# Optimization experiments

Hardware: AMD Instinct MI355X
Metric: run time of the kernel (lower is better)

Reference implementation:

```python
import jax, jax.numpy as jnp
import numpy as np
import math

B, S, D, H = 2, 2048, 1024, 16
DK = D // H  # 64
THETA = 500000.0


def setup_inputs() -> dict:
    key = jax.random.key(0)
    ks = jax.random.split(key, 6)
    x = jax.random.normal(ks[0], (B, S, D), dtype=jnp.float32)
    # RoPE frequencies: inv_freq = theta^{-(2i/dk)}, angles = pos * inv_freq
    inv_freq = 1.0 / (THETA ** (jnp.arange(0, DK, 2, dtype=jnp.float32) / DK))  # [DK/2]
    angles = jnp.arange(S, dtype=jnp.float32)[:, None] * inv_freq[None, :]      # [S, DK/2]
    freqs_cos = jnp.cos(angles)
    freqs_sin = jnp.sin(angles)
    # causal additive mask [B, S, S]: 0 on/below diagonal, -1e9 above
    causal = jnp.tril(jnp.ones((S, S), dtype=bool))
    mask = jnp.where(causal, 0.0, -1e9).astype(jnp.float32)
    mask = jnp.broadcast_to(mask, (B, S, S))
    scale = 0.02
    wq = jax.random.normal(ks[1], (D, D), dtype=jnp.float32) * scale
    wk = jax.random.normal(ks[2], (D, D), dtype=jnp.float32) * scale
    wv = jax.random.normal(ks[3], (D, D), dtype=jnp.float32) * scale
    wo = jax.random.normal(ks[4], (D, D), dtype=jnp.float32) * scale
    return {"x": x, "freqs_cos": freqs_cos, "freqs_sin": freqs_sin,
            "mask": mask, "wq": wq, "wk": wk, "wv": wv, "wo": wo}


def _apply_rope(t, cos, sin):
    # t: [B, S, H, DK]; cos/sin: [S, DK/2]
    tr = t.reshape(*t.shape[:-1], DK // 2, 2)
    t0, t1 = tr[..., 0], tr[..., 1]
    c = cos[None, :, None, :]
    s = sin[None, :, None, :]
    out = jnp.stack([t0 * c - t1 * s, t0 * s + t1 * c], axis=-1)
    return out.reshape(*t.shape)


def reference(x, freqs_cos, freqs_sin, mask, wq, wk, wv, wo):
    b, s, d = x.shape
    # nn.Linear(bias=False): y = x @ W^T, W is [out, in]
    q = jnp.einsum('bsd,ed->bse', x, wq).reshape(b, s, H, DK)
    k = jnp.einsum('bsd,ed->bse', x, wk).reshape(b, s, H, DK)
    v = jnp.einsum('bsd,ed->bse', x, wv).reshape(b, s, H, DK)
    q = _apply_rope(q, freqs_cos, freqs_sin)
    k = _apply_rope(k, freqs_cos, freqs_sin)
    inv_sqrt_dk = 1.0 / math.sqrt(DK)
    # scores: [B, H, S, S]
    scores = jnp.einsum('bqhd,bkhd->bhqk', q, k) * inv_sqrt_dk
    scores = scores + mask[:, None, :, :]
    # NOTE: the original module divides by sqrt(d_k) a SECOND time before softmax
    attn = jax.nn.softmax(scores * inv_sqrt_dk, axis=-1)
    out = jnp.einsum('bhqk,bkhd->bqhd', attn, v).reshape(b, s, d)
    return jnp.einsum('bsd,ed->bse', out, wo)
```

## Files before the change

kernel.cpp:

```cpp
#include <hip/hip_runtime.h>
#include <stdint.h>

#define Bq 2
#define Sq 2048
#define Dq 1024
#define Hq 16
#define DKq 64

typedef unsigned short u16;
typedef __attribute__((ext_vector_type(8))) __bf16 bf8;
typedef __attribute__((ext_vector_type(4))) __bf16 bf4;
typedef __attribute__((ext_vector_type(4))) float fx4;
typedef __attribute__((ext_vector_type(8))) unsigned short us8;
typedef __attribute__((ext_vector_type(4))) unsigned short us4;

__device__ __forceinline__ u16 f2bf(float f) {
    union { float f; unsigned int i; } v; v.f = f;
    unsigned int r = v.i + 0x7FFFu + ((v.i >> 16) & 1u);
    return (u16)(r >> 16);
}

__device__ __forceinline__ void gll16(const void* g, void* l) {
    typedef __attribute__((address_space(1))) void GV;
    typedef __attribute__((address_space(3))) void LV;
    __builtin_amdgcn_global_load_lds((GV*)g, (LV*)l, 16, 0, 0);
}

template<int N> __device__ __forceinline__ void waitv() {
    asm volatile("s_waitcnt vmcnt(%0)" :: "n"(N) : "memory");
}
__device__ __forceinline__ void SB() { __builtin_amdgcn_sched_barrier(0); }

__global__ void __launch_bounds__(256) cvt_all(const float* __restrict__ x,
                                               const float* __restrict__ wq,
                                               const float* __restrict__ wk,
                                               const float* __restrict__ wv,
                                               const float* __restrict__ wo,
                                               u16* __restrict__ ws) {
    int blk = blockIdx.x;
    const float* s;
    u16* d;
    int i;
    if (blk < 4096)      { s = x;  d = ws;           i = blk * 256 + threadIdx.x; }
    else if (blk < 5120) { s = wq; d = ws + 4194304; i = (blk - 4096) * 256 + threadIdx.x; }
    else if (blk < 6144) { s = wk; d = ws + 5242880; i = (blk - 5120) * 256 + threadIdx.x; }
    else if (blk < 7168) { s = wv; d = ws + 6291456; i = (blk - 6144) * 256 + threadIdx.x; }
    else                 { s = wo; d = ws + 7340032; i = (blk - 7168) * 256 + threadIdx.x; }
    float4 v = *(const float4*)(s + (size_t)i * 4);
    us4 o;
    o[0] = f2bf(v.x); o[1] = f2bf(v.y); o[2] = f2bf(v.z); o[3] = f2bf(v.w);
    *(us4*)(d + (size_t)i * 4) = o;
}

template<int MODE>
__global__ void __launch_bounds__(512, 4) gemm_bt(
    const u16* __restrict__ A,
    const u16* __restrict__ W0, const u16* __restrict__ W1, const u16* __restrict__ W2,
    u16* __restrict__ O0, u16* __restrict__ O1, u16* __restrict__ O2,
    float* __restrict__ Of,
    const float* __restrict__ fc, const float* __restrict__ fs)
{
    constexpr int K = 1024;
    constexpr int NT = 32;
    constexpr int BN = MODE ? 256 : 128;
    constexpr int WN = BN / 4;
    constexpr int NJ = WN / 16;
    constexpr int BOPS = BN / 128;
    constexpr int SOPS = 1 + BOPS;
    constexpr int ASZ = 128 * 32;
    constexpr int BSZ = BN * 32;
    __shared__ __align__(16) u16 As[3 * ASZ];
    __shared__ __align__(16) u16 Bs[3 * BSZ];
    const int tid = threadIdx.x;
    const int lane = tid & 63, wid = tid >> 6;
    const int wr = wid >> 2, wc = wid & 3;
    const int fr = lane & 15, fq = lane >> 4;

    int wgid = blockIdx.x;
    int Xc = wgid & 7, jj = wgid >> 3;
    int by, bx, bz;
    if (MODE == 1) {
        int T = Xc * 48 + jj;
        by = T / 12;
        int p = T - by * 12;
        bz = p >> 2; bx = p & 3;
    } else {
        int T = Xc * 32 + jj;
        by = T >> 3; bx = T & 7; bz = 0;
    }
    const int m0 = by * 128, n0 = bx * BN;

    const u16* Wm = W0;
    u16* Ob = O0;
    if (MODE == 1) {
        if (bz == 1)      { Wm = W1; Ob = O1; }
        else if (bz == 2) { Wm = W2; Ob = O2; }
    }

    const int arow = tid >> 2;
    const int scol = (((tid & 3) ^ (arow & 3)) * 8);
    const u16* ga = A  + (size_t)(m0 + arow) * K + scol;
    const u16* gb = Wm + (size_t)(n0 + arow) * K + scol;

    fx4 acc[4][NJ] = {};

    auto STAGE = [&](int t, int b) {
        gll16(ga + t * 32, As + b * ASZ + tid * 8);
        #pragma unroll
        for (int c = 0; c < BOPS; ++c)
            gll16(gb + (size_t)c * 128 * K + t * 32, Bs + b * BSZ + c * 4096 + tid * 8);
    };

    const int kq = (fq ^ (fr & 3)) * 8;

    STAGE(0, 0); STAGE(1, 1); STAGE(2, 2);
    waitv<2 * SOPS>();
    SB(); __builtin_amdgcn_s_barrier(); SB();

    #pragma unroll 1
    for (int t = 0; t < NT; ++t) {
        const u16* Ab = As + (t % 3) * ASZ;
        const u16* Bb = Bs + (t % 3) * BSZ;
        bf8 af[4], bf[NJ];
        #pragma unroll
        for (int mi = 0; mi < 4; ++mi)
            af[mi] = *(const bf8*)(&Ab[(wr * 64 + mi * 16 + fr) * 32 + kq]);
        #pragma unroll
        for (int nj = 0; nj < NJ; ++nj)
            bf[nj] = *(const bf8*)(&Bb[(wc * WN + nj * 16 + fr) * 32 + kq]);
        if (t + 2 < NT) STAGE(t + 2, (t + 2) % 3);
        __builtin_amdgcn_s_setprio(1);
        #pragma unroll
        for (int mi = 0; mi < 4; ++mi)
            #pragma unroll
            for (int nj = 0; nj < NJ; ++nj)
                acc[mi][nj] = __builtin_amdgcn_mfma_f32_16x16x32_bf16(af[mi], bf[nj], acc[mi][nj], 0, 0, 0);
        __builtin_amdgcn_s_setprio(0);
        SB();
        if (t < NT - 2)       { waitv<SOPS>(); }
        else if (t == NT - 2) { waitv<0>(); }
        SB(); __builtin_amdgcn_s_barrier(); SB();
    }

    if (MODE == 0) {
        #pragma unroll
        for (int mi = 0; mi < 4; ++mi)
            #pragma unroll
            for (int nj = 0; nj < NJ; ++nj)
                #pragma unroll
                for (int r = 0; r < 4; ++r) {
                    int m = m0 + wr * 64 + mi * 16 + fq * 4 + r;
                    int n = n0 + wc * WN + nj * 16 + fr;
                    Of[(size_t)m * 1024 + n] = acc[mi][nj][r];
                }
    } else if (bz == 2) {
        #pragma unroll
        for (int mi = 0; mi < 4; ++mi)
            #pragma unroll
            for (int nj = 0; nj < NJ; ++nj) {
                int n = n0 + wc * WN + nj * 16 + fr;
                int mb = m0 + wr * 64 + mi * 16 + fq * 4;
                int b = mb >> 11, s = mb & 2047;
                int h = n >> 6, dk = n & 63;
                bf4 pk;
                #pragma unroll
                for (int r = 0; r < 4; ++r) pk[r] = (__bf16)acc[mi][nj][r];
                *(bf4*)((__bf16*)Ob + (((size_t)(b * Hq + h)) * DKq + dk) * Sq + s) = pk;
            }
    } else {
        #pragma unroll
        for (int mi = 0; mi < 4; ++mi)
            #pragma unroll
            for (int nj = 0; nj < NJ; ++nj) {
                int n = n0 + wc * WN + nj * 16 + fr;
                int h = n >> 6, dk = n & 63;
                int ip = dk >> 1;
                float sgn = (dk & 1) ? 1.f : -1.f;
                #pragma unroll
                for (int r = 0; r < 4; ++r) {
                    int m = m0 + wr * 64 + mi * 16 + fq * 4 + r;
                    int b = m >> 11, s = m & 2047;
                    float v = acc[mi][nj][r];
                    float pv = __shfl_xor(v, 1);
                    float c  = fc[s * 32 + ip];
                    float sn = fs[s * 32 + ip];
                    float o = v * c + sgn * pv * sn;
                    ((__bf16*)Ob)[(((size_t)(b * Hq + h)) * Sq + s) * DKq + dk] = (__bf16)o;
                }
            }
    }
}

__device__ __forceinline__ int swz(int row) { return ((row & 7) ^ ((row >> 3) & 7)) << 4; }

__global__ void __launch_bounds__(512, 4) attn_k(const u16* __restrict__ Q,
                                                 const u16* __restrict__ Kg,
                                                 const u16* __restrict__ Vtg,
                                                 u16* __restrict__ AO) {
    int L = blockIdx.x + 32 * blockIdx.y;
    int X = L & 7, C = L >> 3;
    const int bh = X * 4 + (C & 3);
    const int Qt = 31 - (C >> 2);
    const int b = bh >> 4, h = bh & 15;
    const int tid = threadIdx.x, lane = tid & 63, wid = tid >> 6;
    const int wq4 = wid & 3, par = wid >> 2;
    const int fr = lane & 15, fq = lane >> 4;
    const int swzfr = swz(fr);

    __shared__ __align__(16) u16 Ks[2][64 * 64];
    __shared__ __align__(16) u16 Vs[2][64 * 64];
    __shared__ __align__(16) u16 Ps[8][16 * 64];
    __shared__ float Lx[4][64];

    const u16* Kp = Kg  + (size_t)bh * Sq * 64;
    const u16* Vp = Vtg + (size_t)bh * 64 * Sq;
    const int q0 = Qt * 64;
    const int nt = Qt + 1;
    const int NS = (nt + 1) >> 1;

    bf8 qf0, qf1;
    {
        const u16* Qp = Q + ((size_t)bh * Sq + q0) * 64;
        int qr = wq4 * 16 + fr;
        qf0 = *(const bf8*)(Qp + qr * 64 + fq * 8);
        qf1 = *(const bf8*)(Qp + qr * 64 + fq * 8 + 32);
    }

    fx4 oacc[4] = {};
    float l_loc = 0.f;

    const int srow = tid >> 3;
    const int sce  = (tid & 7) * 8;
    const int ldst = srow * 128 + (((tid & 7) * 16) ^ swz(srow));

    us8 kreg[2], vreg[2];
    #pragma unroll
    for (int c = 0; c < 2; ++c) {
        int t = c < nt ? c : nt - 1;
        kreg[c] = *(const us8*)(Kp + ((size_t)t * 64 + srow) * 64 + sce);
        vreg[c] = *(const us8*)(Vp + (size_t)srow * Sq + t * 64 + sce);
    }
    #pragma unroll
    for (int c = 0; c < 2; ++c) {
        *(us8*)((char*)Ks[c] + ldst) = kreg[c];
        *(us8*)((char*)Vs[c] + ldst) = vreg[c];
    }
    if (NS > 1) {
        #pragma unroll
        for (int c = 0; c < 2; ++c) {
            int t = 2 + c < nt ? 2 + c : nt - 1;
            kreg[c] = *(const us8*)(Kp + ((size_t)t * 64 + srow) * 64 + sce);
            vreg[c] = *(const us8*)(Vp + (size_t)srow * Sq + t * 64 + sce);
        }
    }
    __syncthreads();

    #pragma unroll 1
    for (int sp = 0; sp < NS; ++sp) {
        const int t = 2 * sp + par;
        if (t < nt) {
            const char* Kb = (const char*)Ks[par];
            const char* Vb = (const char*)Vs[par];
            char* Pw = (char*)Ps[wid] + fr * 128;

            fx4 sf[4];
            __builtin_amdgcn_s_setprio(1);
            #pragma unroll
            for (int sj = 0; sj < 4; ++sj) {
                int krow = sj * 16 + fr;
                bf8 kf0 = *(const bf8*)(Kb + krow * 128 + ((fq * 16) ^ swz(krow)));
                bf8 kf1 = *(const bf8*)(Kb + krow * 128 + ((64 + fq * 16) ^ swz(krow)));
                fx4 a = {0.f, 0.f, 0.f, 0.f};
                a = __builtin_amdgcn_mfma_f32_16x16x32_bf16(kf0, qf0, a, 0, 0, 0);
                a = __builtin_amdgcn_mfma_f32_16x16x32_bf16(kf1, qf1, a, 0, 0, 0);
                sf[sj] = a;
            }
            __builtin_amdgcn_s_setprio(0);

            float pv[4][4];
            #pragma unroll
            for (int sj = 0; sj < 4; ++sj)
                #pragma unroll
                for (int r = 0; r < 4; ++r)
                    pv[sj][r] = __expf(sf[sj][r] * 0.015625f);
            if (t == Qt) {
                int ql = wq4 * 16 + fr;
                #pragma unroll
                for (int sj = 0; sj < 4; ++sj)
                    #pragma unroll
                    for (int r = 0; r < 4; ++r)
                        if (sj * 16 + fq * 4 + r > ql) pv[sj][r] = 0.f;
            }
            #pragma unroll
            for (int sj = 0; sj < 4; ++sj) {
                bf4 w;
                #pragma unroll
                for (int r = 0; r < 4; ++r) { w[r] = (__bf16)pv[sj][r]; l_loc += pv[sj][r]; }
                *(bf4*)(Pw + ((sj * 32 + fq * 8) ^ swzfr)) = w;
            }

            __builtin_amdgcn_s_setprio(1);
            #pragma unroll
            for (int kk = 0; kk < 2; ++kk) {
                bf8 pf = *(const bf8*)(Pw + ((kk * 64 + fq * 16) ^ swzfr));
                #pragma unroll
                for (int mf = 0; mf < 4; ++mf) {
                    int vrow = mf * 16 + fr;
                    bf8 vf = *(const bf8*)(Vb + vrow * 128 + ((kk * 64 + fq * 16) ^ swz(vrow)));
                    oacc[mf] = __builtin_amdgcn_mfma_f32_16x16x32_bf16(vf, pf, oacc[mf], 0, 0, 0);
                }
            }
            __builtin_amdgcn_s_setprio(0);
        }
        __syncthreads();
        if (sp + 1 < NS) {
            #pragma unroll
            for (int c = 0; c < 2; ++c) {
                *(us8*)((char*)Ks[c] + ldst) = kreg[c];
                *(us8*)((char*)Vs[c] + ldst) = vreg[c];
            }
            if (sp + 2 < NS) {
                #pragma unroll
                for (int c = 0; c < 2; ++c) {
                    int tt = 2 * (sp + 2) + c; if (tt > nt - 1) tt = nt - 1;
                    kreg[c] = *(const us8*)(Kp + ((size_t)tt * 64 + srow) * 64 + sce);
                    vreg[c] = *(const us8*)(Vp + (size_t)srow * Sq + tt * 64 + sce);
                }
            }
            __syncthreads();
        }
    }

    l_loc += __shfl_xor(l_loc, 16);
    l_loc += __shfl_xor(l_loc, 32);
    if (par == 1) {
        float* ob = (float*)Ps + wq4 * 1024;
        #pragma unroll
        for (int mf = 0; mf < 4; ++mf)
            *(fx4*)(ob + lane * 16 + mf * 4) = oacc[mf];
        Lx[wq4][lane] = l_loc;
    }
    __syncthreads();
    if (par == 0) {
        const float* ob = (float*)Ps + wq4 * 1024;
        float lt = l_loc + Lx[wq4][lane];
        float linv = __builtin_amdgcn_rcpf(lt);
        int s = q0 + wq4 * 16 + fr;
        #pragma unroll
        for (int mf = 0; mf < 4; ++mf) {
            fx4 oh = *(const fx4*)(ob + lane * 16 + mf * 4);
            bf4 pk;
            #pragma unroll
            for (int r = 0; r < 4; ++r) pk[r] = (__bf16)((oacc[mf][r] + oh[r]) * linv);
            *(bf4*)((__bf16*)AO + ((size_t)(b * Sq + s)) * Dq + h * 64 + mf * 16 + fq * 4) = pk;
        }
    }
}

extern "C" void kernel_launch(void* const* d_in, const int* in_sizes, int n_in,
                              void* d_out, int out_size, void* d_ws, size_t ws_size,
                              hipStream_t stream) {
    const float* x  = (const float*)d_in[0];
    const float* fc = (const float*)d_in[1];
    const float* fs = (const float*)d_in[2];
    const float* wq = (const float*)d_in[4];
    const float* wk = (const float*)d_in[5];
    const float* wv = (const float*)d_in[6];
    const float* wo = (const float*)d_in[7];
    float* out = (float*)d_out;

    u16* ws  = (u16*)d_ws;
    u16* xb  = ws;
    u16* wqb = ws + 4194304;
    u16* wkb = ws + 5242880;
    u16* wvb = ws + 6291456;
    u16* wob = ws + 7340032;
    u16* Qb  = ws + 8388608;
    u16* Kb  = ws + 12582912;
    u16* Vb  = ws + 16777216;
    u16* AOb = ws + 20971520;

    cvt_all<<<8192, 256, 0, stream>>>(x, wq, wk, wv, wo, ws);

    gemm_bt<1><<<384, 512, 0, stream>>>(xb, wqb, wkb, wvb, Qb, Kb, Vb, nullptr, fc, fs);

    dim3 g2(32, 32, 1);
    attn_k<<<g2, 512, 0, stream>>>(Qb, Kb, Vb, AOb);

    gemm_bt<0><<<256, 512, 0, stream>>>(AOb, wob, nullptr, nullptr, nullptr, nullptr, nullptr, out, nullptr, nullptr);
}
```

Before: 104.7 us.

## Double query tile per attention block to reuse K/V tiles across two query groups

```diff
diff --git a/kernel.cpp b/kernel.cpp
--- a/kernel.cpp
+++ b/kernel.cpp
@@ -197,37 +197,41 @@
                                                  const u16* __restrict__ Kg,
                                                  const u16* __restrict__ Vtg,
                                                  u16* __restrict__ AO) {
-    int L = blockIdx.x + 32 * blockIdx.y;
-    int X = L & 7, C = L >> 3;
-    const int bh = X * 4 + (C & 3);
-    const int Qt = 31 - (C >> 2);
+    int j = blockIdx.x;
+    int Xc = j & 7;
+    int lightHalf = j >> 8;
+    int C = (j >> 3) & 31;
+    const int bh = Xc * 4 + (C & 3);
+    const int Qt = lightHalf ? (C >> 2) : (15 - (C >> 2));
     const int b = bh >> 4, h = bh & 15;
     const int tid = threadIdx.x, lane = tid & 63, wid = tid >> 6;
-    const int wq4 = wid & 3, par = wid >> 2;
+    const int qh = wid & 3, par = wid >> 2;
     const int fr = lane & 15, fq = lane >> 4;
-    const int swzfr = swz(fr);
+    const int swq0 = ((fr & 7) ^ ((fr >> 3) & 7)) << 4;
+    const int swq1 = ((fr & 7) ^ (((fr >> 3) + 2) & 7)) << 4;
 
     __shared__ __align__(16) u16 Ks[2][64 * 64];
     __shared__ __align__(16) u16 Vs[2][64 * 64];
-    __shared__ __align__(16) u16 Ps[8][16 * 64];
-    __shared__ float Lx[4][64];
+    __shared__ __align__(16) u16 Ps[8][32 * 64];
+    __shared__ float Lx[2][4][64];
 
     const u16* Kp = Kg  + (size_t)bh * Sq * 64;
     const u16* Vp = Vtg + (size_t)bh * 64 * Sq;
-    const int q0 = Qt * 64;
-    const int nt = Qt + 1;
-    const int NS = (nt + 1) >> 1;
-
-    bf8 qf0, qf1;
+    const int q0 = Qt * 128;
+    const int NS = Qt + 1;
+    const int qwb = q0 + qh * 32;
+
+    bf8 qf00, qf01, qf10, qf11;
     {
-        const u16* Qp = Q + ((size_t)bh * Sq + q0) * 64;
-        int qr = wq4 * 16 + fr;
-        qf0 = *(const bf8*)(Qp + qr * 64 + fq * 8);
-        qf1 = *(const bf8*)(Qp + qr * 64 + fq * 8 + 32);
-    }
-
-    fx4 oacc[4] = {};
-    float l_loc = 0.f;
+        const u16* Qp = Q + ((size_t)bh * Sq + qwb) * 64;
+        qf00 = *(const bf8*)(Qp + fr * 64 + fq * 8);
+        qf01 = *(const bf8*)(Qp + fr * 64 + fq * 8 + 32);
+        qf10 = *(const bf8*)(Qp + (16 + fr) * 64 + fq * 8);
+        qf11 = *(const bf8*)(Qp + (16 + fr) * 64 + fq * 8 + 32);
+    }
+
+    fx4 oacc[2][4] = {};
+    float l0 = 0.f, l1 = 0.f;
 
     const int srow = tid >> 3;
     const int sce  = (tid & 7) * 8;
@@ -236,9 +240,8 @@
     us8 kreg[2], vreg[2];
     #pragma unroll
     for (int c = 0; c < 2; ++c) {
-        int t = c < nt ? c : nt - 1;
-        kreg[c] = *(const us8*)(Kp + ((size_t)t * 64 + srow) * 64 + sce);
-        vreg[c] = *(const us8*)(Vp + (size_t)srow * Sq + t * 64 + sce);
+        kreg[c] = *(const us8*)(Kp + ((size_t)c * 64 + srow) * 64 + sce);
+        vreg[c] = *(const us8*)(Vp + (size_t)srow * Sq + c * 64 + sce);
     }
     #pragma unroll
     for (int c = 0; c < 2; ++c) {
@@ -248,9 +251,8 @@
     if (NS > 1) {
         #pragma unroll
         for (int c = 0; c < 2; ++c) {
-            int t = 2 + c < nt ? 2 + c : nt - 1;
-            kreg[c] = *(const us8*)(Kp + ((size_t)t * 64 + srow) * 64 + sce);
-            vreg[c] = *(const us8*)(Vp + (size_t)srow * Sq + t * 64 + sce);
+            kreg[c] = *(const us8*)(Kp + ((size_t)(2 + c) * 64 + srow) * 64 + sce);
+            vreg[c] = *(const us8*)(Vp + (size_t)srow * Sq + (2 + c) * 64 + sce);
         }
     }
     __syncthreads();
@@ -258,59 +260,63 @@
     #pragma unroll 1
     for (int sp = 0; sp < NS; ++sp) {
         const int t = 2 * sp + par;
-        if (t < nt) {
+        if (t * 64 <= qwb + 31) {
             const char* Kb = (const char*)Ks[par];
             const char* Vb = (const char*)Vs[par];
-            char* Pw = (char*)Ps[wid] + fr * 128;
-
-            fx4 sf[4];
-            __builtin_amdgcn_s_setprio(1);
+            char* Pw = (char*)Ps[wid];
+            const int base = qwb - t * 64;
+            const bool dg = (base < 63);
+
             #pragma unroll
             for (int sj = 0; sj < 4; ++sj) {
                 int krow = sj * 16 + fr;
                 bf8 kf0 = *(const bf8*)(Kb + krow * 128 + ((fq * 16) ^ swz(krow)));
                 bf8 kf1 = *(const bf8*)(Kb + krow * 128 + ((64 + fq * 16) ^ swz(krow)));
-                fx4 a = {0.f, 0.f, 0.f, 0.f};
-                a = __builtin_amdgcn_mfma_f32_16x16x32_bf16(kf0, qf0, a, 0, 0, 0);
-                a = __builtin_amdgcn_mfma_f32_16x16x32_bf16(kf1, qf1, a, 0, 0, 0);
-                sf[sj] = a;
-            }
-            __builtin_amdgcn_s_setprio(0);
-
-            float pv[4][4];
-            #pragma unroll
-            for (int sj = 0; sj < 4; ++sj)
-                #pragma unroll
-                for (int r = 0; r < 4; ++r)
-                    pv[sj][r] = __expf(sf[sj][r] * 0.015625f);
-            if (t == Qt) {
-                int ql = wq4 * 16 + fr;
-                #pragma unroll
-                for (int sj = 0; sj < 4; ++sj)
+                __builtin_amdgcn_s_setprio(1);
+                fx4 s0 = {0.f, 0.f, 0.f, 0.f}, s1 = {0.f, 0.f, 0.f, 0.f};
+                s0 = __builtin_amdgcn_mfma_f32_16x16x32_bf16(kf0, qf00, s0, 0, 0, 0);
+                s0 = __builtin_amdgcn_mfma_f32_16x16x32_bf16(kf1, qf01, s0, 0, 0, 0);
+                s1 = __builtin_amdgcn_mfma_f32_16x16x32_bf16(kf0, qf10, s1, 0, 0, 0);
+                s1 = __builtin_amdgcn_mfma_f32_16x16x32_bf16(kf1, qf11, s1, 0, 0, 0);
+                __builtin_amdgcn_s_setprio(0);
+                float p0[4], p1[4];
+                #pragma unroll
+                for (int r = 0; r < 4; ++r) {
+                    p0[r] = __expf(s0[r] * 0.015625f);
+                    p1[r] = __expf(s1[r] * 0.015625f);
+                }
+                if (dg) {
                     #pragma unroll
-                    for (int r = 0; r < 4; ++r)
-                        if (sj * 16 + fq * 4 + r > ql) pv[sj][r] = 0.f;
-            }
-            #pragma unroll
-            for (int sj = 0; sj < 4; ++sj) {
-                bf4 w;
-                #pragma unroll
-                for (int r = 0; r < 4; ++r) { w[r] = (__bf16)pv[sj][r]; l_loc += pv[sj][r]; }
-                *(bf4*)(Pw + ((sj * 32 + fq * 8) ^ swzfr)) = w;
-            }
-
-            __builtin_amdgcn_s_setprio(1);
+                    for (int r = 0; r < 4; ++r) {
+                        int kvr = sj * 16 + fq * 4 + r;
+                        if (kvr > base + fr)      p0[r] = 0.f;
+                        if (kvr > base + 16 + fr) p1[r] = 0.f;
+                    }
+                }
+                bf4 w0, w1;
+                #pragma unroll
+                for (int r = 0; r < 4; ++r) {
+                    w0[r] = (__bf16)p0[r]; l0 += p0[r];
+                    w1[r] = (__bf16)p1[r]; l1 += p1[r];
+                }
+                *(bf4*)(Pw + fr * 128 + ((sj * 32 + fq * 8) ^ swq0)) = w0;
+                *(bf4*)(Pw + (16 + fr) * 128 + ((sj * 32 + fq * 8) ^ swq1)) = w1;
+            }
+
             #pragma unroll
             for (int kk = 0; kk < 2; ++kk) {
-                bf8 pf = *(const bf8*)(Pw + ((kk * 64 + fq * 16) ^ swzfr));
+                bf8 pf0 = *(const bf8*)(Pw + fr * 128 + ((kk * 64 + fq * 16) ^ swq0));
+                bf8 pf1 = *(const bf8*)(Pw + (16 + fr) * 128 + ((kk * 64 + fq * 16) ^ swq1));
+                __builtin_amdgcn_s_setprio(1);
                 #pragma unroll
                 for (int mf = 0; mf < 4; ++mf) {
                     int vrow = mf * 16 + fr;
                     bf8 vf = *(const bf8*)(Vb + vrow * 128 + ((kk * 64 + fq * 16) ^ swz(vrow)));
-                    oacc[mf] = __builtin_amdgcn_mfma_f32_16x16x32_bf16(vf, pf, oacc[mf], 0, 0, 0);
-                }
-            }
-            __builtin_amdgcn_s_setprio(0);
+                    oacc[0][mf] = __builtin_amdgcn_mfma_f32_16x16x32_bf16(vf, pf0, oacc[0][mf], 0, 0, 0);
+                    oacc[1][mf] = __builtin_amdgcn_mfma_f32_16x16x32_bf16(vf, pf1, oacc[1][mf], 0, 0, 0);
+                }
+                __builtin_amdgcn_s_setprio(0);
+            }
         }
         __syncthreads();
         if (sp + 1 < NS) {
@@ -322,7 +328,7 @@
             if (sp + 2 < NS) {
                 #pragma unroll
                 for (int c = 0; c < 2; ++c) {
-                    int tt = 2 * (sp + 2) + c; if (tt > nt - 1) tt = nt - 1;
+                    int tt = 2 * (sp + 2) + c;
                     kreg[c] = *(const us8*)(Kp + ((size_t)tt * 64 + srow) * 64 + sce);
                     vreg[c] = *(const us8*)(Vp + (size_t)srow * Sq + tt * 64 + sce);
                 }
@@ -331,28 +337,38 @@
         }
     }
 
-    l_loc += __shfl_xor(l_loc, 16);
-    l_loc += __shfl_xor(l_loc, 32);
+    l0 += __shfl_xor(l0, 16); l0 += __shfl_xor(l0, 32);
+    l1 += __shfl_xor(l1, 16); l1 += __shfl_xor(l1, 32);
     if (par == 1) {
-        float* ob = (float*)Ps + wq4 * 1024;
-        #pragma unroll
-        for (int mf = 0; mf < 4; ++mf)
-            *(fx4*)(ob + lane * 16 + mf * 4) = oacc[mf];
-        Lx[wq4][lane] = l_loc;
+        float* pb = (float*)Ps + qh * 2048;
+        #pragma unroll
+        for (int qs = 0; qs < 2; ++qs)
+            #pragma unroll
+            for (int mf = 0; mf < 4; ++mf) {
+                int slot = (qs * 4 + mf) ^ (lane & 7);
+                *(fx4*)(pb + lane * 32 + slot * 4) = oacc[qs][mf];
+            }
+        Lx[0][qh][lane] = l0;
+        Lx[1][qh][lane] = l1;
     }
     __syncthreads();
     if (par == 0) {
-        const float* ob = (float*)Ps + wq4 * 1024;
-        float lt = l_loc + Lx[wq4][lane];
-        float linv = __builtin_amdgcn_rcpf(lt);
-        int s = q0 + wq4 * 16 + fr;
-        #pragma unroll
-        for (int mf = 0; mf < 4; ++mf) {
-            fx4 oh = *(const fx4*)(ob + lane * 16 + mf * 4);
-            bf4 pk;
-            #pragma unroll
-            for (int r = 0; r < 4; ++r) pk[r] = (__bf16)((oacc[mf][r] + oh[r]) * linv);
-            *(bf4*)((__bf16*)AO + ((size_t)(b * Sq + s)) * Dq + h * 64 + mf * 16 + fq * 4) = pk;
+        const float* pb = (const float*)Ps + qh * 2048;
+        float li0 = __builtin_amdgcn_rcpf(l0 + Lx[0][qh][lane]);
+        float li1 = __builtin_amdgcn_rcpf(l1 + Lx[1][qh][lane]);
+        #pragma unroll
+        for (int qs = 0; qs < 2; ++qs) {
+            float li = qs ? li1 : li0;
+            int s = q0 + qh * 32 + qs * 16 + fr;
+            #pragma unroll
+            for (int mf = 0; mf < 4; ++mf) {
+                int slot = (qs * 4 + mf) ^ (lane & 7);
+                fx4 oh = *(const fx4*)(pb + lane * 32 + slot * 4);
+                bf4 pk;
+                #pragma unroll
+                for (int r = 0; r < 4; ++r) pk[r] = (__bf16)((oacc[qs][mf][r] + oh[r]) * li);
+                *(bf4*)((__bf16*)AO + ((size_t)(b * Sq + s)) * Dq + h * 64 + mf * 16 + fq * 4) = pk;
+            }
         }
     }
 }
@@ -384,8 +400,7 @@
 
     gemm_bt<1><<<384, 512, 0, stream>>>(xb, wqb, wkb, wvb, Qb, Kb, Vb, nullptr, fc, fs);
 
-    dim3 g2(32, 32, 1);
-    attn_k<<<g2, 512, 0, stream>>>(Qb, Kb, Vb, AOb);
+    attn_k<<<512, 512, 0, stream>>>(Qb, Kb, Vb, AOb);
 
     gemm_bt<0><<<256, 512, 0, stream>>>(AOb, wob, nullptr, nullptr, nullptr, nullptr, nullptr, out, nullptr, nullptr);
 }
```

New measurement: 144.5 us. +37.9%, slower.

## Fuse fp32-to-bf16 conversion of x into the QKV projection GEMM

Applied to the files above, without the earlier changes.

```diff
diff --git a/kernel.cpp b/kernel.cpp
--- a/kernel.cpp
+++ b/kernel.cpp
@@ -31,21 +31,19 @@
 }
 __device__ __forceinline__ void SB() { __builtin_amdgcn_sched_barrier(0); }
 
-__global__ void __launch_bounds__(256) cvt_all(const float* __restrict__ x,
-                                               const float* __restrict__ wq,
-                                               const float* __restrict__ wk,
-                                               const float* __restrict__ wv,
-                                               const float* __restrict__ wo,
-                                               u16* __restrict__ ws) {
+__global__ void __launch_bounds__(256) cvt_w(const float* __restrict__ wq,
+                                             const float* __restrict__ wk,
+                                             const float* __restrict__ wv,
+                                             const float* __restrict__ wo,
+                                             u16* __restrict__ ws) {
     int blk = blockIdx.x;
     const float* s;
     u16* d;
     int i;
-    if (blk < 4096)      { s = x;  d = ws;           i = blk * 256 + threadIdx.x; }
-    else if (blk < 5120) { s = wq; d = ws + 4194304; i = (blk - 4096) * 256 + threadIdx.x; }
-    else if (blk < 6144) { s = wk; d = ws + 5242880; i = (blk - 5120) * 256 + threadIdx.x; }
-    else if (blk < 7168) { s = wv; d = ws + 6291456; i = (blk - 6144) * 256 + threadIdx.x; }
-    else                 { s = wo; d = ws + 7340032; i = (blk - 7168) * 256 + threadIdx.x; }
+    if (blk < 1024)      { s = wq; d = ws + 4194304; i = blk * 256 + threadIdx.x; }
+    else if (blk < 2048) { s = wk; d = ws + 5242880; i = (blk - 1024) * 256 + threadIdx.x; }
+    else if (blk < 3072) { s = wv; d = ws + 6291456; i = (blk - 2048) * 256 + threadIdx.x; }
+    else                 { s = wo; d = ws + 7340032; i = (blk - 3072) * 256 + threadIdx.x; }
     float4 v = *(const float4*)(s + (size_t)i * 4);
     us4 o;
     o[0] = f2bf(v.x); o[1] = f2bf(v.y); o[2] = f2bf(v.z); o[3] = f2bf(v.w);
@@ -54,7 +52,7 @@
 
 template<int MODE>
 __global__ void __launch_bounds__(512, 4) gemm_bt(
-    const u16* __restrict__ A,
+    const u16* __restrict__ A, const float* __restrict__ Af,
     const u16* __restrict__ W0, const u16* __restrict__ W1, const u16* __restrict__ W2,
     u16* __restrict__ O0, u16* __restrict__ O1, u16* __restrict__ O2,
     float* __restrict__ Of,
@@ -66,7 +64,6 @@
     constexpr int WN = BN / 4;
     constexpr int NJ = WN / 16;
     constexpr int BOPS = BN / 128;
-    constexpr int SOPS = 1 + BOPS;
     constexpr int ASZ = 128 * 32;
     constexpr int BSZ = BN * 32;
     __shared__ __align__(16) u16 As[3 * ASZ];
@@ -98,47 +95,82 @@
     }
 
     const int arow = tid >> 2;
-    const int scol = (((tid & 3) ^ (arow & 3)) * 8);
-    const u16* ga = A  + (size_t)(m0 + arow) * K + scol;
-    const u16* gb = Wm + (size_t)(n0 + arow) * K + scol;
+    const int sw = ((tid & 3) ^ (arow & 3)) * 8;
+    const u16*   ga  = A  + (size_t)(m0 + arow) * K + sw;
+    const float* gaf = Af + (size_t)(m0 + arow) * K + (tid & 3) * 8;
+    const u16*   gb  = Wm + (size_t)(n0 + arow) * K + sw;
 
     fx4 acc[4][NJ] = {};
 
-    auto STAGE = [&](int t, int b) {
-        gll16(ga + t * 32, As + b * ASZ + tid * 8);
+    auto STAGE_B = [&](int t, int b) {
         #pragma unroll
         for (int c = 0; c < BOPS; ++c)
             gll16(gb + (size_t)c * 128 * K + t * 32, Bs + b * BSZ + c * 4096 + tid * 8);
     };
+    auto STAGE_A0 = [&](int t, int b) {
+        gll16(ga + t * 32, As + b * ASZ + tid * 8);
+    };
+    float4 xra, xrb;
+    auto LOAD_X = [&](int t) {
+        xra = *(const float4*)(gaf + t * 32);
+        xrb = *(const float4*)(gaf + t * 32 + 4);
+    };
+    auto WRITE_A = [&](int b) {
+        us8 w;
+        w[0] = f2bf(xra.x); w[1] = f2bf(xra.y); w[2] = f2bf(xra.z); w[3] = f2bf(xra.w);
+        w[4] = f2bf(xrb.x); w[5] = f2bf(xrb.y); w[6] = f2bf(xrb.z); w[7] = f2bf(xrb.w);
+        *(us8*)(As + b * ASZ + arow * 32 + sw) = w;
+    };
 
     const int kq = (fq ^ (fr & 3)) * 8;
 
-    STAGE(0, 0); STAGE(1, 1); STAGE(2, 2);
-    waitv<2 * SOPS>();
+    if (MODE == 1) {
+        LOAD_X(0); WRITE_A(0);
+        LOAD_X(1);
+        STAGE_B(0, 0); STAGE_B(1, 1); STAGE_B(2, 2);
+        waitv<4>();
+        asm volatile("s_waitcnt lgkmcnt(0)" ::: "memory");
+    } else {
+        STAGE_A0(0, 0); STAGE_B(0, 0);
+        STAGE_A0(1, 1); STAGE_B(1, 1);
+        STAGE_A0(2, 2); STAGE_B(2, 2);
+        waitv<4>();
+    }
     SB(); __builtin_amdgcn_s_barrier(); SB();
 
     #pragma unroll 1
     for (int t = 0; t < NT; ++t) {
         const u16* Ab = As + (t % 3) * ASZ;
         const u16* Bb = Bs + (t % 3) * BSZ;
-        bf8 af[4], bf[NJ];
+        bf8 af[4], bfv[NJ];
         #pragma unroll
         for (int mi = 0; mi < 4; ++mi)
             af[mi] = *(const bf8*)(&Ab[(wr * 64 + mi * 16 + fr) * 32 + kq]);
         #pragma unroll
         for (int nj = 0; nj < NJ; ++nj)
-            bf[nj] = *(const bf8*)(&Bb[(wc * WN + nj * 16 + fr) * 32 + kq]);
-        if (t + 2 < NT) STAGE(t + 2, (t + 2) % 3);
+            bfv[nj] = *(const bf8*)(&Bb[(wc * WN + nj * 16 + fr) * 32 + kq]);
+        if (MODE == 1) {
+            if (t + 1 < NT) WRITE_A((t + 1) % 3);
+            if (t + 2 < NT) { LOAD_X(t + 2); STAGE_B(t + 2, (t + 2) % 3); }
+        } else {
+            if (t + 2 < NT) { STAGE_A0(t + 2, (t + 2) % 3); STAGE_B(t + 2, (t + 2) % 3); }
+        }
         __builtin_amdgcn_s_setprio(1);
         #pragma unroll
         for (int mi = 0; mi < 4; ++mi)
             #pragma unroll
             for (int nj = 0; nj < NJ; ++nj)
-                acc[mi][nj] = __builtin_amdgcn_mfma_f32_16x16x32_bf16(af[mi], bf[nj], acc[mi][nj], 0, 0, 0);
+                acc[mi][nj] = __builtin_amdgcn_mfma_f32_16x16x32_bf16(af[mi], bfv[nj], acc[mi][nj], 0, 0, 0);
         __builtin_amdgcn_s_setprio(0);
         SB();
-        if (t < NT - 2)       { waitv<SOPS>(); }
-        else if (t == NT - 2) { waitv<0>(); }
+        if (MODE == 1) {
+            if (t < NT - 2)       { waitv<4>(); }
+            else if (t == NT - 2) { waitv<0>(); }
+            asm volatile("s_waitcnt lgkmcnt(0)" ::: "memory");
+        } else {
+            if (t < NT - 2)       { waitv<2>(); }
+            else if (t == NT - 2) { waitv<0>(); }
+        }
         SB(); __builtin_amdgcn_s_barrier(); SB();
     }
 
@@ -370,7 +402,6 @@
     float* out = (float*)d_out;
 
     u16* ws  = (u16*)d_ws;
-    u16* xb  = ws;
     u16* wqb = ws + 4194304;
     u16* wkb = ws + 5242880;
     u16* wvb = ws + 6291456;
@@ -380,12 +411,14 @@
     u16* Vb  = ws + 16777216;
     u16* AOb = ws + 20971520;
 
-    cvt_all<<<8192, 256, 0, stream>>>(x, wq, wk, wv, wo, ws);
-
-    gemm_bt<1><<<384, 512, 0, stream>>>(xb, wqb, wkb, wvb, Qb, Kb, Vb, nullptr, fc, fs);
+    cvt_w<<<4096, 256, 0, stream>>>(wq, wk, wv, wo, ws);
+
+    gemm_bt<1><<<384, 512, 0, stream>>>(nullptr, x, wqb, wkb, wvb,
+                                        Qb, Kb, Vb, nullptr, fc, fs);
 
     dim3 g2(32, 32, 1);
     attn_k<<<g2, 512, 0, stream>>>(Qb, Kb, Vb, AOb);
 
-    gemm_bt<0><<<256, 512, 0, stream>>>(AOb, wob, nullptr, nullptr, nullptr, nullptr, nullptr, out, nullptr, nullptr);
-}
+    gemm_bt<0><<<256, 512, 0, stream>>>(AOb, nullptr, wob, nullptr, nullptr,
+                                        nullptr, nullptr, nullptr, out, nullptr, nullptr);
+}
```

Result: slower. 108.1 us (+3.2%).
